# Performance work log

Hardware: AMD Instinct MI355X
Metric: run time of the kernel (lower is better)

Reference implementation:

```python
import jax, jax.numpy as jnp
import numpy as np

B, L, T = 512, 512, 128


def setup_inputs() -> dict:
    key = jax.random.key(0)
    k0, k1, k2, k3, k4 = jax.random.split(key, 5)
    input_tensors = jax.random.normal(k0, (B, L, T), dtype=jnp.float32)
    # xavier_normal_ for square [T, T]: std = sqrt(2 / (T + T))
    transitions = jax.random.normal(k1, (T, T), dtype=jnp.float32) * np.sqrt(2.0 / (T + T)).astype(np.float32)
    start_transitions = jax.random.normal(k2, (T,), dtype=jnp.float32)
    end_transitions = jax.random.normal(k3, (T,), dtype=jnp.float32)
    label_tensors = jax.random.randint(k4, (B, L), 0, T)
    mask_tensors = jnp.ones((B, L), dtype=jnp.int32)
    return {
        "input_tensors": input_tensors,
        "transitions": transitions,
        "start_transitions": start_transitions,
        "end_transitions": end_transitions,
        "label_tensors": label_tensors,
        "mask_tensors": mask_tensors,
    }


def _crf_nll(input_tensors, transitions, start_transitions, end_transitions,
             label_tensors, mask_tensors):
    maskf = mask_tensors.astype(jnp.float32)  # [B, L]
    # ---------- log-partition (denominator): forward algorithm via scan ----------
    emits = jnp.swapaxes(input_tensors, 0, 1)  # [L, B, T]
    mt = jnp.swapaxes(maskf, 0, 1)             # [L, B]
    alpha0 = start_transitions[None, :] + emits[0]  # [B, T]

    def step(alpha, xs):
        emit_t, m_t = xs  # [B, T], [B]
        # inner[b, i, j] = alpha[b, i] + transitions[i, j] + emit_t[b, j]
        inner = alpha[:, :, None] + transitions[None, :, :] + emit_t[:, None, :]
        new_alpha = jax.nn.logsumexp(inner, axis=1)  # [B, T]
        alpha = new_alpha * m_t[:, None] + alpha * (1.0 - m_t)[:, None]
        return alpha, None

    alpha, _ = jax.lax.scan(step, alpha0, (emits[1:], mt[1:]))
    log_denominator = jax.nn.logsumexp(alpha + end_transitions[None, :], axis=-1)  # [B]

    # ---------- joint (numerator): gold-path score, fully vectorized ----------
    score = start_transitions[label_tensors[:, 0]]  # [B]
    # transition scores between consecutive gold tags, masked by mask[t+1]
    trans_sc = transitions[label_tensors[:, :-1], label_tensors[:, 1:]]  # [B, L-1]
    # emission scores for steps 0..L-2, masked by mask[t]
    emit_sc = jnp.take_along_axis(input_tensors[:, :-1, :], label_tensors[:, :-1, None], axis=2)[..., 0]  # [B, L-1]
    score = score + jnp.sum(trans_sc * maskf[:, 1:] + emit_sc * maskf[:, :-1], axis=1)
    # last valid tag per sequence
    last_idx = maskf.sum(axis=1).astype(jnp.int32) - 1  # [B]
    last_tags = jnp.take_along_axis(label_tensors, last_idx[:, None], axis=1)[:, 0]  # [B]
    last_input_sc = jnp.take_along_axis(input_tensors[:, -1, :], last_tags[:, None], axis=1)[:, 0]  # [B]
    score = score + end_transitions[last_tags] + last_input_sc * maskf[:, -1]

    return jnp.sum(log_denominator - score) / maskf.sum()


def reference(input_tensors, transitions, start_transitions, end_transitions,
              label_tensors, mask_tensors):
    return _crf_nll(input_tensors, transitions, start_transitions, end_transitions,
                    label_tensors, mask_tensors)
```

## Files before the change

kernel.cpp:

```cpp
#include <hip/hip_runtime.h>
#include <hip/hip_bf16.h>

#define Bc 512
#define Lc 512
#define Tc 128
#define GB 16
#define NW 8
#define PSTR 136
#define PBUF (GB * PSTR)

typedef __attribute__((ext_vector_type(8))) short bf16x8;
typedef __attribute__((ext_vector_type(4))) float f32x4;

__device__ __forceinline__ void bar_lgkm() {
  asm volatile("s_waitcnt lgkmcnt(0)\n\ts_barrier" ::: "memory");
}
__device__ __forceinline__ unsigned short f2bf_u(float f) {
  __hip_bfloat16 h = __float2bfloat16(f);
  unsigned short us;
  __builtin_memcpy(&us, &h, 2);
  return us;
}
__device__ __forceinline__ short f2bf(float f) { return (short)f2bf_u(f); }

__global__ __launch_bounds__(512, 1)
void crf_forward(const float* __restrict__ x,
                 const float* __restrict__ trans,
                 const float* __restrict__ startT,
                 const float* __restrict__ endT,
                 const int*   __restrict__ labels,
                 const int*   __restrict__ mask,
                 float* __restrict__ diff_out,
                 float* __restrict__ msum_out)
{
  __shared__ __align__(16) unsigned short Pl[2 * PBUF];
  __shared__ __align__(16) float r_s[GB];
  __shared__ unsigned char anyz[Lc];
  __shared__ __align__(16) float c_s[GB];
  __shared__ float score_s[GB];
  __shared__ float msum_s[GB];
  __shared__ float red[GB][NW];

  const int tid  = threadIdx.x;
  const int lane = tid & 63;
  const int w    = tid >> 6;
  const int crow = lane & 15;
  const int khi  = lane >> 4;
  const int bg0  = blockIdx.x * GB;
  const int jloc = 16 * w + crow;

  if (tid < Lc) {
    unsigned zz = 0;
    for (int bb = 0; bb < GB; ++bb)
      zz |= (unsigned)(mask[(size_t)(bg0 + bb) * Lc + tid] == 0);
    anyz[tid] = (unsigned char)zz;
  }

  for (int bb = 2 * w; bb < 2 * w + 2; ++bb) {
    const int bglob = bg0 + bb;
    const int* lbp = labels + (size_t)bglob * Lc;
    const int* mkp = mask + (size_t)bglob * Lc;
    const float* xrow = x + (size_t)bglob * Lc * Tc;
    float sp = 0.f, msp = 0.f;
    for (int t = lane; t < Lc; t += 64) {
      int l0 = lbp[t];
      int m0 = mkp[t];
      msp += (float)m0;
      if (t < Lc - 1) {
        int l1 = lbp[t + 1];
        float m1 = (float)mkp[t + 1];
        sp += trans[l0 * Tc + l1] * m1 + xrow[(size_t)t * Tc + l0] * (float)m0;
      }
    }
#pragma unroll
    for (int off = 32; off; off >>= 1) {
      sp += __shfl_xor(sp, off);
      msp += __shfl_xor(msp, off);
    }
    if (lane == 0) {
      int last_idx = (int)msp - 1;
      int lt = lbp[last_idx];
      score_s[bb] = sp + startT[lbp[0]] + endT[lt]
                  + xrow[(size_t)(Lc - 1) * Tc + lt] * (float)mkp[Lc - 1];
      msum_s[bb] = msp;
    }
  }

  bf16x8 Bf0, Bf1, Bf2, Bf3;
  {
    const float* tp_ = trans + jloc;
#pragma unroll
    for (int e = 0; e < 8; ++e) Bf0[e] = f2bf(__expf(tp_[(8 * khi + e) * Tc]));
#pragma unroll
    for (int e = 0; e < 8; ++e) Bf1[e] = f2bf(__expf(tp_[(32 + 8 * khi + e) * Tc]));
#pragma unroll
    for (int e = 0; e < 8; ++e) Bf2[e] = f2bf(__expf(tp_[(64 + 8 * khi + e) * Tc]));
#pragma unroll
    for (int e = 0; e < 8; ++e) Bf3[e] = f2bf(__expf(tp_[(96 + 8 * khi + e) * Tc]));
  }

  const int aoff = crow * PSTR + 8 * khi;
  const int woff = (4 * khi) * PSTR + jloc;
  const float* xp0 = x + (size_t)(bg0 + 4 * khi + 0) * Lc * Tc + jloc;
  const float* xp1 = x + (size_t)(bg0 + 4 * khi + 1) * Lc * Tc + jloc;
  const float* xp2 = x + (size_t)(bg0 + 4 * khi + 2) * Lc * Tc + jloc;
  const float* xp3 = x + (size_t)(bg0 + 4 * khi + 3) * Lc * Tc + jloc;
  const bool rlane = (w == 0) && (crow == 0);

  __syncthreads();

  float st_j = startT[jloc];
  float a00 = st_j + xp0[0];
  float a01 = st_j + xp1[0];
  float a02 = st_j + xp2[0];
  float a03 = st_j + xp3[0];
  if (rlane) {
    f32x4 cv = {a00, a01, a02, a03};
    *(f32x4*)&r_s[khi << 2] = cv;
  }
  __syncthreads();
  f32x4 cb = *(const f32x4*)&r_s[khi << 2];
  float Ao0 = __expf(a00 - cb.x);
  float Ao1 = __expf(a01 - cb.y);
  float Ao2 = __expf(a02 - cb.z);
  float Ao3 = __expf(a03 - cb.w);
  Pl[PBUF + woff + 0 * PSTR] = f2bf_u(Ao0);
  Pl[PBUF + woff + 1 * PSTR] = f2bf_u(Ao1);
  Pl[PBUF + woff + 2 * PSTR] = f2bf_u(Ao2);
  Pl[PBUF + woff + 3 * PSTR] = f2bf_u(Ao3);
  f32x4 c  = rlane ? cb : (f32x4){0.f, 0.f, 0.f, 0.f};
  f32x4 lr = {0.f, 0.f, 0.f, 0.f};
  __syncthreads();
  if (rlane) {
    f32x4 one = {1.f, 1.f, 1.f, 1.f};
    *(f32x4*)&r_s[khi << 2] = one;
  }
  float xA0 = xp0[1 * Tc], xA1 = xp1[1 * Tc], xA2 = xp2[1 * Tc], xA3 = xp3[1 * Tc];
  float xB0 = xp0[2 * Tc], xB1 = xp1[2 * Tc], xB2 = xp2[2 * Tc], xB3 = xp3[2 * Tc];
  __syncthreads();

#define MFMA_(A, B, C_) C_ = __builtin_amdgcn_mfma_f32_16x16x32_bf16(A, B, C_, 0, 0, 0)
#define STEP(T, RB, WB, PH, XA0, XA1, XA2, XA3) do {                           \
    bf16x8 Af0 = *(const bf16x8*)&Pl[(RB) * PBUF + aoff +  0];                 \
    bf16x8 Af1 = *(const bf16x8*)&Pl[(RB) * PBUF + aoff + 32];                 \
    bf16x8 Af2 = *(const bf16x8*)&Pl[(RB) * PBUF + aoff + 64];                 \
    bf16x8 Af3 = *(const bf16x8*)&Pl[(RB) * PBUF + aoff + 96];                 \
    unsigned char az = anyz[T];                                                \
    float ex0 = __expf(XA0), ex1 = __expf(XA1);                                \
    float ex2 = __expf(XA2), ex3 = __expf(XA3);                                \
    { int tp__ = (T) + 2; if (tp__ > Lc - 1) tp__ = Lc - 1;                    \
      size_t xo__ = (size_t)tp__ * Tc;                                         \
      XA0 = xp0[xo__]; XA1 = xp1[xo__]; XA2 = xp2[xo__]; XA3 = xp3[xo__]; }    \
    f32x4 Ca = {0.f, 0.f, 0.f, 0.f};                                           \
    f32x4 Cb2 = {0.f, 0.f, 0.f, 0.f};                                          \
    MFMA_(Af0, Bf0, Ca);  MFMA_(Af2, Bf2, Cb2);                                \
    MFMA_(Af1, Bf1, Ca);  MFMA_(Af3, Bf3, Cb2);                                \
    f32x4 Cr = Ca + Cb2;                                                       \
    float v0, v1, v2, v3;                                                      \
    if ((PH) == 1) {                                                           \
      f32x4 rr = *(const f32x4*)&r_s[khi << 2];                                \
      v0 = Cr.x * rr.x * ex0; v1 = Cr.y * rr.y * ex1;                          \
      v2 = Cr.z * rr.z * ex2; v3 = Cr.w * rr.w * ex3;                          \
    } else {                                                                   \
      v0 = Cr.x * ex0; v1 = Cr.y * ex1;                                        \
      v2 = Cr.z * ex2; v3 = Cr.w * ex3;                                        \
    }                                                                          \
    if (az) {                                      \
      int m0 = mask[(size_t)(bg0 + 4 * khi + 0) * Lc + (T)];                   \
      int m1 = mask[(size_t)(bg0 + 4 * khi + 1) * Lc + (T)];                   \
      int m2 = mask[(size_t)(bg0 + 4 * khi + 2) * Lc + (T)];                   \
      int m3 = mask[(size_t)(bg0 + 4 * khi + 3) * Lc + (T)];                   \
      Ao0 = m0 ? v0 : Ao0; Ao1 = m1 ? v1 : Ao1;                                \
      Ao2 = m2 ? v2 : Ao2; Ao3 = m3 ? v3 : Ao3;                                \
      if ((PH) == 1 && rlane) {                                                \
        c.x += m0 ? lr.x : 0.f; c.y += m1 ? lr.y : 0.f;                        \
        c.z += m2 ? lr.z : 0.f; c.w += m3 ? lr.w : 0.f;                        \
      }                                                                        \
    } else {                                                                   \
      Ao0 = v0; Ao1 = v1; Ao2 = v2; Ao3 = v3;                                  \
      if ((PH) == 1 && rlane) {                                                \
        c.x += lr.x; c.y += lr.y; c.z += lr.z; c.w += lr.w;                    \
      }                                                                        \
    }                                                                          \
    Pl[(WB) * PBUF + woff + 0 * PSTR] = f2bf_u(Ao0);                           \
    Pl[(WB) * PBUF + woff + 1 * PSTR] = f2bf_u(Ao1);                           \
    Pl[(WB) * PBUF + woff + 2 * PSTR] = f2bf_u(Ao2);                           \
    Pl[(WB) * PBUF + woff + 3 * PSTR] = f2bf_u(Ao3);                           \
    if ((PH) == 0 && rlane) {           \
      int E0 = (int)((__float_as_uint(Ao0) >> 23) & 0xffu) - 127;              \
      int E1 = (int)((__float_as_uint(Ao1) >> 23) & 0xffu) - 127;              \
      int E2 = (int)((__float_as_uint(Ao2) >> 23) & 0xffu) - 127;              \
      int E3 = (int)((__float_as_uint(Ao3) >> 23) & 0xffu) - 127;              \
      lr.x = (float)E0 * 0.6931471805599453f;                                  \
      lr.y = (float)E1 * 0.6931471805599453f;                                  \
      lr.z = (float)E2 * 0.6931471805599453f;                                  \
      lr.w = (float)E3 * 0.6931471805599453f;                                  \
      f32x4 rv;                                                                \
      rv.x = __uint_as_float((unsigned)(127 - E0) << 23);                      \
      rv.y = __uint_as_float((unsigned)(127 - E1) << 23);                      \
      rv.z = __uint_as_float((unsigned)(127 - E2) << 23);                      \
      rv.w = __uint_as_float((unsigned)(127 - E3) << 23);                      \
      *(f32x4*)&r_s[khi << 2] = rv;                                            \
    }                                                                          \
    bar_lgkm();                                                                \
  } while (0)

  for (int t = 1; t <= Lc - 4; t += 4) {
    STEP(t,     1, 0, 1, xA0, xA1, xA2, xA3);
    STEP(t + 1, 0, 1, 2, xB0, xB1, xB2, xB3);
    STEP(t + 2, 1, 0, 2, xA0, xA1, xA2, xA3);
    STEP(t + 3, 0, 1, 0, xB0, xB1, xB2, xB3);
  }
  STEP(Lc - 3, 1, 0, 1, xA0, xA1, xA2, xA3);
  STEP(Lc - 2, 0, 1, 2, xB0, xB1, xB2, xB3);
  STEP(Lc - 1, 1, 0, 2, xA0, xA1, xA2, xA3);
#undef STEP
#undef MFMA_

  if (rlane) *(f32x4*)&c_s[khi << 2] = c;
  float eex = __expf(endT[jloc]);
  float s0 = Ao0 * eex, s1 = Ao1 * eex, s2 = Ao2 * eex, s3 = Ao3 * eex;
#pragma unroll
  for (int off = 1; off < 16; off <<= 1) {
    s0 += __shfl_xor(s0, off);
    s1 += __shfl_xor(s1, off);
    s2 += __shfl_xor(s2, off);
    s3 += __shfl_xor(s3, off);
  }
  if (crow == 0) {
    red[4 * khi + 0][w] = s0;
    red[4 * khi + 1][w] = s1;
    red[4 * khi + 2][w] = s2;
    red[4 * khi + 3][w] = s3;
  }
  __syncthreads();
  if (tid < GB) {
    float tot = 0.f;
#pragma unroll
    for (int ww = 0; ww < NW; ++ww) tot += red[tid][ww];
    float logZ = c_s[tid] + __logf(tot);
    diff_out[bg0 + tid] = logZ - score_s[tid];
    msum_out[bg0 + tid] = msum_s[tid];
  }
}

__global__ __launch_bounds__(512)
void crf_final(const float* __restrict__ diff, const float* __restrict__ msum,
               float* __restrict__ out)
{
  __shared__ float sd[512];
  __shared__ float sm[512];
  int t = threadIdx.x;
  sd[t] = diff[t];
  sm[t] = msum[t];
  __syncthreads();
  for (int s = 256; s > 0; s >>= 1) {
    if (t < s) { sd[t] += sd[t + s]; sm[t] += sm[t + s]; }
    __syncthreads();
  }
  if (t == 0) out[0] = sd[0] / sm[0];
}

extern "C" void kernel_launch(void* const* d_in, const int* in_sizes, int n_in,
                              void* d_out, int out_size, void* d_ws, size_t ws_size,
                              hipStream_t stream) {
  const float* x      = (const float*)d_in[0];
  const float* trans  = (const float*)d_in[1];
  const float* startT = (const float*)d_in[2];
  const float* endT   = (const float*)d_in[3];
  const int*   labels = (const int*)d_in[4];
  const int*   mask   = (const int*)d_in[5];
  float* out = (float*)d_out;
  float* ws  = (float*)d_ws;
  float* diff = ws;
  float* msum = ws + Bc;

  crf_forward<<<dim3(Bc / GB), dim3(512), 0, stream>>>(
      x, trans, startT, endT, labels, mask, diff, msum);
  crf_final<<<dim3(1), dim3(512), 0, stream>>>(diff, msum, out);
}
```

Before: 197.9 us.

## Transpose MFMA operands so each lane owns one batch row with vector loads

Swaps the MFMA operand roles so the exp(transitions) fragments become the A operand and the alpha state becomes the B operand. In the new mapping each lane handles one batch row and four consecutive tags. The padded LDS stride is replaced by an XOR-swizzled layout. Emission loads, the bf16 state writes and the mask reads become single vector or scalar accesses instead of four strided ones, and the rescale bookkeeping drops from four values per lane to one. The intent is fewer global and LDS instructions per serial time step, with some added risk from the swizzle indexing and the changed lane mapping.

Result: faster. 171.8 us (-13.2%).

```diff
diff --git a/kernel.cpp b/kernel.cpp
--- a/kernel.cpp
+++ b/kernel.cpp
@@ -6,11 +6,10 @@
 #define Tc 128
 #define GB 16
 #define NW 8
-#define PSTR 136
-#define PBUF (GB * PSTR)
 
 typedef __attribute__((ext_vector_type(8))) short bf16x8;
 typedef __attribute__((ext_vector_type(4))) float f32x4;
+typedef __attribute__((ext_vector_type(2))) unsigned u32x2;
 
 __device__ __forceinline__ void bar_lgkm() {
   asm volatile("s_waitcnt lgkmcnt(0)\n\ts_barrier" ::: "memory");
@@ -22,6 +21,9 @@
   return us;
 }
 __device__ __forceinline__ short f2bf(float f) { return (short)f2bf_u(f); }
+__device__ __forceinline__ unsigned pk2(float a, float b) {
+  return (unsigned)f2bf_u(a) | ((unsigned)f2bf_u(b) << 16);
+}
 
 __global__ __launch_bounds__(512, 1)
 void crf_forward(const float* __restrict__ x,
@@ -33,7 +35,7 @@
                  float* __restrict__ diff_out,
                  float* __restrict__ msum_out)
 {
-  __shared__ __align__(16) unsigned short Pl[2 * PBUF];
+  __shared__ __align__(16) unsigned short Pl[2][GB * Tc];
   __shared__ __align__(16) float r_s[GB];
   __shared__ unsigned char anyz[Lc];
   __shared__ __align__(16) float c_s[GB];
@@ -47,7 +49,7 @@
   const int crow = lane & 15;
   const int khi  = lane >> 4;
   const int bg0  = blockIdx.x * GB;
-  const int jloc = 16 * w + crow;
+  const bool rl  = (w == 0) && (khi == 0);
 
   if (tid < Lc) {
     unsigned zz = 0;
@@ -86,153 +88,117 @@
     }
   }
 
-  bf16x8 Bf0, Bf1, Bf2, Bf3;
+  bf16x8 Ef0, Ef1, Ef2, Ef3;
   {
-    const float* tp_ = trans + jloc;
-#pragma unroll
-    for (int e = 0; e < 8; ++e) Bf0[e] = f2bf(__expf(tp_[(8 * khi + e) * Tc]));
-#pragma unroll
-    for (int e = 0; e < 8; ++e) Bf1[e] = f2bf(__expf(tp_[(32 + 8 * khi + e) * Tc]));
-#pragma unroll
-    for (int e = 0; e < 8; ++e) Bf2[e] = f2bf(__expf(tp_[(64 + 8 * khi + e) * Tc]));
-#pragma unroll
-    for (int e = 0; e < 8; ++e) Bf3[e] = f2bf(__expf(tp_[(96 + 8 * khi + e) * Tc]));
-  }
-
-  const int aoff = crow * PSTR + 8 * khi;
-  const int woff = (4 * khi) * PSTR + jloc;
-  const float* xp0 = x + (size_t)(bg0 + 4 * khi + 0) * Lc * Tc + jloc;
-  const float* xp1 = x + (size_t)(bg0 + 4 * khi + 1) * Lc * Tc + jloc;
-  const float* xp2 = x + (size_t)(bg0 + 4 * khi + 2) * Lc * Tc + jloc;
-  const float* xp3 = x + (size_t)(bg0 + 4 * khi + 3) * Lc * Tc + jloc;
-  const bool rlane = (w == 0) && (crow == 0);
-
-  __syncthreads();
-
-  float st_j = startT[jloc];
-  float a00 = st_j + xp0[0];
-  float a01 = st_j + xp1[0];
-  float a02 = st_j + xp2[0];
-  float a03 = st_j + xp3[0];
-  if (rlane) {
-    f32x4 cv = {a00, a01, a02, a03};
-    *(f32x4*)&r_s[khi << 2] = cv;
-  }
-  __syncthreads();
-  f32x4 cb = *(const f32x4*)&r_s[khi << 2];
-  float Ao0 = __expf(a00 - cb.x);
-  float Ao1 = __expf(a01 - cb.y);
-  float Ao2 = __expf(a02 - cb.z);
-  float Ao3 = __expf(a03 - cb.w);
-  Pl[PBUF + woff + 0 * PSTR] = f2bf_u(Ao0);
-  Pl[PBUF + woff + 1 * PSTR] = f2bf_u(Ao1);
-  Pl[PBUF + woff + 2 * PSTR] = f2bf_u(Ao2);
-  Pl[PBUF + woff + 3 * PSTR] = f2bf_u(Ao3);
-  f32x4 c  = rlane ? cb : (f32x4){0.f, 0.f, 0.f, 0.f};
-  f32x4 lr = {0.f, 0.f, 0.f, 0.f};
-  __syncthreads();
-  if (rlane) {
-    f32x4 one = {1.f, 1.f, 1.f, 1.f};
-    *(f32x4*)&r_s[khi << 2] = one;
-  }
-  float xA0 = xp0[1 * Tc], xA1 = xp1[1 * Tc], xA2 = xp2[1 * Tc], xA3 = xp3[1 * Tc];
-  float xB0 = xp0[2 * Tc], xB1 = xp1[2 * Tc], xB2 = xp2[2 * Tc], xB3 = xp3[2 * Tc];
+    const int jr = 16 * w + crow;
+#pragma unroll
+    for (int e = 0; e < 8; ++e) Ef0[e] = f2bf(__expf(trans[(     8 * khi + e) * Tc + jr]));
+#pragma unroll
+    for (int e = 0; e < 8; ++e) Ef1[e] = f2bf(__expf(trans[(32 + 8 * khi + e) * Tc + jr]));
+#pragma unroll
+    for (int e = 0; e < 8; ++e) Ef2[e] = f2bf(__expf(trans[(64 + 8 * khi + e) * Tc + jr]));
+#pragma unroll
+    for (int e = 0; e < 8; ++e) Ef3[e] = f2bf(__expf(trans[(96 + 8 * khi + e) * Tc + jr]));
+  }
+
+  const int sw   = (crow & 7) << 3;
+  const int boff = crow * Tc;
+  const int ro0  = boff + (( 0 + 8 * khi) ^ sw);
+  const int ro1  = boff + ((32 + 8 * khi) ^ sw);
+  const int ro2  = boff + ((64 + 8 * khi) ^ sw);
+  const int ro3  = boff + ((96 + 8 * khi) ^ sw);
+  const int wo   = boff + ((16 * w + 4 * khi) ^ sw);
+  const float* xp = x + (size_t)(bg0 + crow) * Lc * Tc + 16 * w + 4 * khi;
+  const int*   mkl = mask + (size_t)(bg0 + crow) * Lc;
+
+  __syncthreads();
+
+  f32x4 st4 = *(const f32x4*)&startT[16 * w + 4 * khi];
+  f32x4 a0  = st4 + *(const f32x4*)xp;
+  if (rl) r_s[crow] = a0.x;
+  __syncthreads();
+  float cb = r_s[crow];
+  f32x4 Ao;
+  Ao.x = __expf(a0.x - cb); Ao.y = __expf(a0.y - cb);
+  Ao.z = __expf(a0.z - cb); Ao.w = __expf(a0.w - cb);
+  {
+    u32x2 pv = {pk2(Ao.x, Ao.y), pk2(Ao.z, Ao.w)};
+    *(u32x2*)&Pl[1][wo] = pv;
+  }
+  float c  = rl ? cb : 0.f;
+  float lr = 0.f;
+  __syncthreads();
+  if (rl) r_s[crow] = 1.f;
+  f32x4 xA = *(const f32x4*)(xp + 1 * Tc);
+  f32x4 xB = *(const f32x4*)(xp + 2 * Tc);
   __syncthreads();
 
 #define MFMA_(A, B, C_) C_ = __builtin_amdgcn_mfma_f32_16x16x32_bf16(A, B, C_, 0, 0, 0)
-#define STEP(T, RB, WB, PH, XA0, XA1, XA2, XA3) do {                           \
-    bf16x8 Af0 = *(const bf16x8*)&Pl[(RB) * PBUF + aoff +  0];                 \
-    bf16x8 Af1 = *(const bf16x8*)&Pl[(RB) * PBUF + aoff + 32];                 \
-    bf16x8 Af2 = *(const bf16x8*)&Pl[(RB) * PBUF + aoff + 64];                 \
-    bf16x8 Af3 = *(const bf16x8*)&Pl[(RB) * PBUF + aoff + 96];                 \
+#define STEP(T, RB, WB, PH, XQ) do {                                           \
+    bf16x8 Bf0 = *(const bf16x8*)&Pl[RB][ro0];                                 \
+    bf16x8 Bf1 = *(const bf16x8*)&Pl[RB][ro1];                                 \
+    bf16x8 Bf2 = *(const bf16x8*)&Pl[RB][ro2];                                 \
+    bf16x8 Bf3 = *(const bf16x8*)&Pl[RB][ro3];                                 \
     unsigned char az = anyz[T];                                                \
-    float ex0 = __expf(XA0), ex1 = __expf(XA1);                                \
-    float ex2 = __expf(XA2), ex3 = __expf(XA3);                                \
+    f32x4 ex;                                                                  \
+    ex.x = __expf(XQ.x); ex.y = __expf(XQ.y);                                  \
+    ex.z = __expf(XQ.z); ex.w = __expf(XQ.w);                                  \
     { int tp__ = (T) + 2; if (tp__ > Lc - 1) tp__ = Lc - 1;                    \
-      size_t xo__ = (size_t)tp__ * Tc;                                         \
-      XA0 = xp0[xo__]; XA1 = xp1[xo__]; XA2 = xp2[xo__]; XA3 = xp3[xo__]; }    \
+      XQ = *(const f32x4*)(xp + (size_t)tp__ * Tc); }                          \
     f32x4 Ca = {0.f, 0.f, 0.f, 0.f};                                           \
     f32x4 Cb2 = {0.f, 0.f, 0.f, 0.f};                                          \
-    MFMA_(Af0, Bf0, Ca);  MFMA_(Af2, Bf2, Cb2);                                \
-    MFMA_(Af1, Bf1, Ca);  MFMA_(Af3, Bf3, Cb2);                                \
+    MFMA_(Ef0, Bf0, Ca);  MFMA_(Ef2, Bf2, Cb2);                                \
+    MFMA_(Ef1, Bf1, Ca);  MFMA_(Ef3, Bf3, Cb2);                                \
     f32x4 Cr = Ca + Cb2;                                                       \
-    float v0, v1, v2, v3;                                                      \
+    f32x4 v;                                                                   \
     if ((PH) == 1) {                                                           \
-      f32x4 rr = *(const f32x4*)&r_s[khi << 2];                                \
-      v0 = Cr.x * rr.x * ex0; v1 = Cr.y * rr.y * ex1;                          \
-      v2 = Cr.z * rr.z * ex2; v3 = Cr.w * rr.w * ex3;                          \
+      float rr = r_s[crow];                                                    \
+      v.x = Cr.x * rr * ex.x; v.y = Cr.y * rr * ex.y;                          \
+      v.z = Cr.z * rr * ex.z; v.w = Cr.w * rr * ex.w;                          \
     } else {                                                                   \
-      v0 = Cr.x * ex0; v1 = Cr.y * ex1;                                        \
-      v2 = Cr.z * ex2; v3 = Cr.w * ex3;                                        \
-    }                                                                          \
-    if (az) {                                      \
-      int m0 = mask[(size_t)(bg0 + 4 * khi + 0) * Lc + (T)];                   \
-      int m1 = mask[(size_t)(bg0 + 4 * khi + 1) * Lc + (T)];                   \
-      int m2 = mask[(size_t)(bg0 + 4 * khi + 2) * Lc + (T)];                   \
-      int m3 = mask[(size_t)(bg0 + 4 * khi + 3) * Lc + (T)];                   \
-      Ao0 = m0 ? v0 : Ao0; Ao1 = m1 ? v1 : Ao1;                                \
-      Ao2 = m2 ? v2 : Ao2; Ao3 = m3 ? v3 : Ao3;                                \
-      if ((PH) == 1 && rlane) {                                                \
-        c.x += m0 ? lr.x : 0.f; c.y += m1 ? lr.y : 0.f;                        \
-        c.z += m2 ? lr.z : 0.f; c.w += m3 ? lr.w : 0.f;                        \
-      }                                                                        \
+      v.x = Cr.x * ex.x; v.y = Cr.y * ex.y;                                    \
+      v.z = Cr.z * ex.z; v.w = Cr.w * ex.w;                                    \
+    }                                                                          \
+    if (az) {    \
+      int m = mkl[T];                                                          \
+      Ao.x = m ? v.x : Ao.x; Ao.y = m ? v.y : Ao.y;                            \
+      Ao.z = m ? v.z : Ao.z; Ao.w = m ? v.w : Ao.w;                            \
+      if ((PH) == 1 && rl) c += m ? lr : 0.f;                                  \
     } else {                                                                   \
-      Ao0 = v0; Ao1 = v1; Ao2 = v2; Ao3 = v3;                                  \
-      if ((PH) == 1 && rlane) {                                                \
-        c.x += lr.x; c.y += lr.y; c.z += lr.z; c.w += lr.w;                    \
-      }                                                                        \
-    }                                                                          \
-    Pl[(WB) * PBUF + woff + 0 * PSTR] = f2bf_u(Ao0);                           \
-    Pl[(WB) * PBUF + woff + 1 * PSTR] = f2bf_u(Ao1);                           \
-    Pl[(WB) * PBUF + woff + 2 * PSTR] = f2bf_u(Ao2);                           \
-    Pl[(WB) * PBUF + woff + 3 * PSTR] = f2bf_u(Ao3);                           \
-    if ((PH) == 0 && rlane) {           \
-      int E0 = (int)((__float_as_uint(Ao0) >> 23) & 0xffu) - 127;              \
-      int E1 = (int)((__float_as_uint(Ao1) >> 23) & 0xffu) - 127;              \
-      int E2 = (int)((__float_as_uint(Ao2) >> 23) & 0xffu) - 127;              \
-      int E3 = (int)((__float_as_uint(Ao3) >> 23) & 0xffu) - 127;              \
-      lr.x = (float)E0 * 0.6931471805599453f;                                  \
-      lr.y = (float)E1 * 0.6931471805599453f;                                  \
-      lr.z = (float)E2 * 0.6931471805599453f;                                  \
-      lr.w = (float)E3 * 0.6931471805599453f;                                  \
-      f32x4 rv;                                                                \
-      rv.x = __uint_as_float((unsigned)(127 - E0) << 23);                      \
-      rv.y = __uint_as_float((unsigned)(127 - E1) << 23);                      \
-      rv.z = __uint_as_float((unsigned)(127 - E2) << 23);                      \
-      rv.w = __uint_as_float((unsigned)(127 - E3) << 23);                      \
-      *(f32x4*)&r_s[khi << 2] = rv;                                            \
+      Ao = v;                                                                  \
+      if ((PH) == 1 && rl) c += lr;                                            \
+    }                                                                          \
+    {                                                                          \
+      u32x2 pv = {pk2(Ao.x, Ao.y), pk2(Ao.z, Ao.w)};                           \
+      *(u32x2*)&Pl[WB][wo] = pv;                                               \
+    }                                                                          \
+    if ((PH) == 0 && rl) {            \
+      int E0 = (int)((__float_as_uint(Ao.x) >> 23) & 0xffu) - 127;             \
+      lr = (float)E0 * 0.6931471805599453f;                                    \
+      r_s[crow] = __uint_as_float((unsigned)(127 - E0) << 23);                 \
     }                                                                          \
     bar_lgkm();                                                                \
   } while (0)
 
   for (int t = 1; t <= Lc - 4; t += 4) {
-    STEP(t,     1, 0, 1, xA0, xA1, xA2, xA3);
-    STEP(t + 1, 0, 1, 2, xB0, xB1, xB2, xB3);
-    STEP(t + 2, 1, 0, 2, xA0, xA1, xA2, xA3);
-    STEP(t + 3, 0, 1, 0, xB0, xB1, xB2, xB3);
-  }
-  STEP(Lc - 3, 1, 0, 1, xA0, xA1, xA2, xA3);
-  STEP(Lc - 2, 0, 1, 2, xB0, xB1, xB2, xB3);
-  STEP(Lc - 1, 1, 0, 2, xA0, xA1, xA2, xA3);
+    STEP(t,     1, 0, 1, xA);
+    STEP(t + 1, 0, 1, 2, xB);
+    STEP(t + 2, 1, 0, 2, xA);
+    STEP(t + 3, 0, 1, 0, xB);
+  }
+  STEP(Lc - 3, 1, 0, 1, xA);
+  STEP(Lc - 2, 0, 1, 2, xB);
+  STEP(Lc - 1, 1, 0, 2, xA);
 #undef STEP
 #undef MFMA_
 
-  if (rlane) *(f32x4*)&c_s[khi << 2] = c;
-  float eex = __expf(endT[jloc]);
-  float s0 = Ao0 * eex, s1 = Ao1 * eex, s2 = Ao2 * eex, s3 = Ao3 * eex;
-#pragma unroll
-  for (int off = 1; off < 16; off <<= 1) {
-    s0 += __shfl_xor(s0, off);
-    s1 += __shfl_xor(s1, off);
-    s2 += __shfl_xor(s2, off);
-    s3 += __shfl_xor(s3, off);
-  }
-  if (crow == 0) {
-    red[4 * khi + 0][w] = s0;
-    red[4 * khi + 1][w] = s1;
-    red[4 * khi + 2][w] = s2;
-    red[4 * khi + 3][w] = s3;
-  }
+  if (rl) c_s[crow] = c;
+  f32x4 ev = *(const f32x4*)&endT[16 * w + 4 * khi];
+  float part = Ao.x * __expf(ev.x) + Ao.y * __expf(ev.y)
+             + Ao.z * __expf(ev.z) + Ao.w * __expf(ev.w);
+  part += __shfl_xor(part, 16);
+  part += __shfl_xor(part, 32);
+  if (khi == 0) red[crow][w] = part;
   __syncthreads();
   if (tid < GB) {
     float tot = 0.f;
```
